# Kernel optimization log

Measured on AMD Instinct MI355X. Metric: run time of the kernel, lower is better.

## Reference

```python
import jax, jax.numpy as jnp
import numpy as np

B, C, H, W = 8, 256, 128, 128
HEADS, DIM_HEAD = 4, 32
HID = HEADS * DIM_HEAD  # 128


def setup_inputs() -> dict:
    key = jax.random.key(0)
    k1, k2, k3, k4 = jax.random.split(key, 4)
    x = jax.random.normal(k1, (B, C, H, W), dtype=jnp.float32)
    # 1x1 conv weights stored as [out_ch, in_ch]
    w_qkv = jax.random.normal(k2, (3 * HID, C), dtype=jnp.float32) * (1.0 / np.sqrt(C))
    w_out = jax.random.normal(k3, (C, HID), dtype=jnp.float32) * (1.0 / np.sqrt(HID))
    b_out = jax.random.normal(k4, (C,), dtype=jnp.float32) * 0.01
    return {"x": x, "w_qkv": w_qkv, "w_out": w_out, "b_out": b_out}


def reference(x, w_qkv, w_out, b_out):
    b, c, h, w = x.shape
    n = h * w
    # 1x1 conv == channel matmul
    qkv = jnp.einsum('oc,bchw->bohw', w_qkv, x)  # [b, 3*HID, h, w]
    q, k, v = jnp.split(qkv, 3, axis=1)
    # rearrange 'b (heads d) h w -> b heads d (h w)'
    def to_heads(t):
        return t.reshape(b, HEADS, DIM_HEAD, n)
    q, k, v = to_heads(q), to_heads(k), to_heads(v)
    k = jax.nn.softmax(k, axis=-1)  # over spatial n
    # q_scale is False: q used as-is
    context = jnp.einsum('bhdn,bhen->bhde', k, v)   # [b, heads, d, e] small
    out = jnp.einsum('bhde,bhdn->bhen', context, q)  # [b, heads, e, n]
    out = out.reshape(b, HID, h, w)
    out = jnp.einsum('oc,bchw->bohw', w_out, out) + b_out[None, :, None, None]
    return out
```

## Files before the change

### kernel.cpp

```cpp
#include <hip/hip_runtime.h>
#include <stdint.h>

#define BB 8
#define CIN 256
#define NSP 16384
#define HID 128

typedef __bf16 bfrag __attribute__((ext_vector_type(8)));
typedef float  f32x4 __attribute__((ext_vector_type(4)));

__device__ __forceinline__ unsigned short f2bf(float f) {
  union { float f; unsigned int u; } v; v.f = f;
  unsigned int u = v.u;
  return (unsigned short)((u + 0x7FFFu + ((u >> 16) & 1u)) >> 16);
}

__global__ __launch_bounds__(512, 2) void la_fused(const float* __restrict__ x,
                                                   const float* __restrict__ w_qkv,
                                                   unsigned short* __restrict__ qT,
                                                   float* __restrict__ ctxp,
                                                   float* __restrict__ sums) {
  __shared__ __align__(16) union {
    struct { unsigned short Wt[384][40]; unsigned short Xb[128][40]; } g;
    struct { unsigned short Lk[64][136]; unsigned short Lv[64][136];
             float Pc[4][1024]; } e;
  } sh;
  const int chunk = blockIdx.x;
  const int n0 = chunk * 128;
  const int b = blockIdx.y;
  const int t = threadIdx.x;
  const int lane = t & 63, wv = t >> 6;
  const int l15 = lane & 15, q = lane >> 4;
  const int cl = t & 31;
  const int n16 = (t >> 5) * 8;
  const float* xp = x + (size_t)b * CIN * NSP + n0;
  f32x4 acc[3][8];
#pragma unroll
  for (int i = 0; i < 3; ++i)
#pragma unroll
    for (int j = 0; j < 8; ++j) acc[i][j] = 0.0f;

  for (int kc = 0; kc < 8; ++kc) {
#pragma unroll
    for (int i = 0; i < 3; ++i) {
      const int id = t + i * 512;
      const int row = id >> 2, c8 = (id & 3) * 8;
      const float* wr = w_qkv + (size_t)row * CIN + kc * 32 + c8;
      const float4 wa = *(const float4*)wr;
      const float4 wb4 = *(const float4*)(wr + 4);
      ushort4 p0, p1;
      p0.x = f2bf(wa.x); p0.y = f2bf(wa.y); p0.z = f2bf(wa.z); p0.w = f2bf(wa.w);
      p1.x = f2bf(wb4.x); p1.y = f2bf(wb4.y); p1.z = f2bf(wb4.z); p1.w = f2bf(wb4.w);
      *(ushort4*)&sh.g.Wt[row][c8] = p0;
      *(ushort4*)&sh.g.Wt[row][c8 + 4] = p1;
    }
    const float* xr = xp + (size_t)(kc * 32 + cl) * NSP + n16;
    const float4 xa = *(const float4*)xr;
    const float4 xb4 = *(const float4*)(xr + 4);
    sh.g.Xb[n16 + 0][cl] = f2bf(xa.x);
    sh.g.Xb[n16 + 1][cl] = f2bf(xa.y);
    sh.g.Xb[n16 + 2][cl] = f2bf(xa.z);
    sh.g.Xb[n16 + 3][cl] = f2bf(xa.w);
    sh.g.Xb[n16 + 4][cl] = f2bf(xb4.x);
    sh.g.Xb[n16 + 5][cl] = f2bf(xb4.y);
    sh.g.Xb[n16 + 6][cl] = f2bf(xb4.z);
    sh.g.Xb[n16 + 7][cl] = f2bf(xb4.w);
    __syncthreads();
    bfrag a0 = *(const bfrag*)&sh.g.Wt[wv * 16 + l15][q * 8];
    bfrag a1 = *(const bfrag*)&sh.g.Wt[128 + wv * 16 + l15][q * 8];
    bfrag a2 = *(const bfrag*)&sh.g.Wt[256 + wv * 16 + l15][q * 8];
    bfrag bb[8];
#pragma unroll
    for (int ni = 0; ni < 8; ++ni) bb[ni] = *(const bfrag*)&sh.g.Xb[ni * 16 + l15][q * 8];
#pragma unroll
    for (int ni = 0; ni < 8; ++ni) {
      acc[0][ni] = __builtin_amdgcn_mfma_f32_16x16x32_bf16(a0, bb[ni], acc[0][ni], 0, 0, 0);
      acc[1][ni] = __builtin_amdgcn_mfma_f32_16x16x32_bf16(a1, bb[ni], acc[1][ni], 0, 0, 0);
      acc[2][ni] = __builtin_amdgcn_mfma_f32_16x16x32_bf16(a2, bb[ni], acc[2][ni], 0, 0, 0);
    }
    __syncthreads();
  }

  {
    unsigned short* qb = qT + (size_t)b * NSP * HID;
    const int qrow = wv * 16 + q * 4;
#pragma unroll
    for (int ni = 0; ni < 8; ++ni) {
      const int n = n0 + ni * 16 + l15;
      ushort4 pk;
      pk.x = f2bf(acc[0][ni][0]);
      pk.y = f2bf(acc[0][ni][1]);
      pk.z = f2bf(acc[0][ni][2]);
      pk.w = f2bf(acc[0][ni][3]);
      *(ushort4*)(qb + (size_t)n * HID + qrow) = pk;
    }
  }
  {
    float sp[4] = {0.f, 0.f, 0.f, 0.f};
#pragma unroll
    for (int ni = 0; ni < 8; ++ni)
#pragma unroll
      for (int rg = 0; rg < 4; ++rg) sp[rg] += __expf(acc[1][ni][rg]);
#pragma unroll
    for (int rg = 0; rg < 4; ++rg) {
      float s = sp[rg];
      s += __shfl_down(s, 8, 16);
      s += __shfl_down(s, 4, 16);
      s += __shfl_down(s, 2, 16);
      s += __shfl_down(s, 1, 16);
      if (l15 == 0) atomicAdd(&sums[b * 128 + wv * 16 + q * 4 + rg], s);
    }
  }
  float* cp = ctxp + ((size_t)chunk * 32 + b * 4) * 1024;
#pragma unroll
  for (int ph = 0; ph < 2; ++ph) {
    if ((wv >> 2) == ph) {
      const int r = (wv & 3) * 16 + q * 4;
#pragma unroll
      for (int ni = 0; ni < 8; ++ni)
#pragma unroll
        for (int rg = 0; rg < 4; ++rg) {
          sh.e.Lk[r + rg][ni * 16 + l15] = f2bf(__expf(acc[1][ni][rg]));
          sh.e.Lv[r + rg][ni * 16 + l15] = f2bf(acc[2][ni][rg]);
        }
    }
    __syncthreads();
    const int hl = wv >> 2, nq = wv & 3;
    f32x4 c2[2][2];
    c2[0][0] = 0.f; c2[0][1] = 0.f; c2[1][0] = 0.f; c2[1][1] = 0.f;
    bfrag ka[2], vb[2];
#pragma unroll
    for (int d2 = 0; d2 < 2; ++d2)
      ka[d2] = *(const bfrag*)&sh.e.Lk[hl * 32 + d2 * 16 + l15][nq * 32 + q * 8];
#pragma unroll
    for (int e2 = 0; e2 < 2; ++e2)
      vb[e2] = *(const bfrag*)&sh.e.Lv[hl * 32 + e2 * 16 + l15][nq * 32 + q * 8];
#pragma unroll
    for (int d2 = 0; d2 < 2; ++d2)
#pragma unroll
      for (int e2 = 0; e2 < 2; ++e2)
        c2[d2][e2] = __builtin_amdgcn_mfma_f32_16x16x32_bf16(ka[d2], vb[e2], c2[d2][e2], 0, 0, 0);
    const int slot = hl * 2 + (nq & 1);
    if (nq < 2) {
#pragma unroll
      for (int d2 = 0; d2 < 2; ++d2)
#pragma unroll
        for (int e2 = 0; e2 < 2; ++e2)
#pragma unroll
          for (int rg = 0; rg < 4; ++rg)
            sh.e.Pc[slot][(d2 * 16 + q * 4 + rg) * 32 + e2 * 16 + l15] = c2[d2][e2][rg];
    }
    __syncthreads();
    if (nq >= 2) {
#pragma unroll
      for (int d2 = 0; d2 < 2; ++d2)
#pragma unroll
        for (int e2 = 0; e2 < 2; ++e2)
#pragma unroll
          for (int rg = 0; rg < 4; ++rg)
            sh.e.Pc[slot][(d2 * 16 + q * 4 + rg) * 32 + e2 * 16 + l15] += c2[d2][e2][rg];
    }
    __syncthreads();
    for (int idx = t; idx < 2048; idx += 512) {
      const int h2 = idx >> 10, pos = idx & 1023;
      cp[(ph * 2 + h2) * 1024 + pos] = sh.e.Pc[h2 * 2][pos] + sh.e.Pc[h2 * 2 + 1][pos];
    }
    __syncthreads();
  }
}

__global__ __launch_bounds__(256) void la_reduce(const float* __restrict__ ctxp,
                                                 float* __restrict__ ctxu) {
  const int gid = blockIdx.x * 256 + threadIdx.x;
  float s = 0.f;
#pragma unroll 8
  for (int c = 0; c < 128; ++c) s += ctxp[(size_t)c * 32768 + gid];
  ctxu[gid] = s;
}

__global__ __launch_bounds__(128) void la_weff(const float* __restrict__ w_out,
                                               const float* __restrict__ ctxu,
                                               const float* __restrict__ sums,
                                               unsigned short* __restrict__ weff) {
  const int o = blockIdx.x;
  const int b = blockIdx.y;
  const int cp = threadIdx.x;
  const int h = cp >> 5, d = cp & 31;
  const float* wrow = w_out + (size_t)o * HID + h * 32;
  const float* crow = ctxu + ((size_t)(b * 4 + h) * 32 + d) * 32;
  float s = 0.f;
#pragma unroll 8
  for (int e = 0; e < 32; ++e) s += wrow[e] * crow[e];
  s *= (1.0f / sums[b * 128 + h * 32 + d]);
  weff[((size_t)b * 256 + o) * HID + cp] = f2bf(s);
}

__global__ __launch_bounds__(256) void la_out_gemm(const unsigned short* __restrict__ weff,
                                                   const unsigned short* __restrict__ qT,
                                                   const float* __restrict__ b_out,
                                                   float* __restrict__ out) {
  __shared__ __align__(16) unsigned short At[128][40];
  __shared__ __align__(16) unsigned short Bt[128][40];
  const int mblk = blockIdx.x;
  const int n0 = blockIdx.y * 128;
  const int b = blockIdx.z;
  const int t = threadIdx.x;
  const int lane = t & 63, wv = t >> 6;
  const int wm = (wv >> 1) * 64, wn = (wv & 1) * 64;
  const int l15 = lane & 15, q = lane >> 4;
  f32x4 acc[4][4];
#pragma unroll
  for (int i = 0; i < 4; ++i)
#pragma unroll
    for (int j = 0; j < 4; ++j) acc[i][j] = 0.0f;
  const unsigned short* abase = weff + ((size_t)b * 256 + mblk * 128) * HID;
  const unsigned short* bbase = qT + ((size_t)b * NSP + n0) * HID;
  const int r = t >> 1, hh = (t & 1) * 16;
  for (int kc = 0; kc < 4; ++kc) {
    const int ko = kc * 32 + hh;
    uint4 a0 = *(const uint4*)(abase + (size_t)r * HID + ko);
    uint4 a1 = *(const uint4*)(abase + (size_t)r * HID + ko + 8);
    uint4 b0 = *(const uint4*)(bbase + (size_t)r * HID + ko);
    uint4 b1 = *(const uint4*)(bbase + (size_t)r * HID + ko + 8);
    *(uint4*)&At[r][hh] = a0;
    *(uint4*)&At[r][hh + 8] = a1;
    *(uint4*)&Bt[r][hh] = b0;
    *(uint4*)&Bt[r][hh + 8] = b1;
    __syncthreads();
    bfrag a[4], bf[4];
#pragma unroll
    for (int mi = 0; mi < 4; ++mi) a[mi] = *(const bfrag*)&At[wm + mi * 16 + l15][q * 8];
#pragma unroll
    for (int ni = 0; ni < 4; ++ni) bf[ni] = *(const bfrag*)&Bt[wn + ni * 16 + l15][q * 8];
#pragma unroll
    for (int mi = 0; mi < 4; ++mi)
#pragma unroll
      for (int ni = 0; ni < 4; ++ni)
        acc[mi][ni] = __builtin_amdgcn_mfma_f32_16x16x32_bf16(a[mi], bf[ni], acc[mi][ni], 0, 0, 0);
    __syncthreads();
  }
  float* obase = out + ((size_t)b * 256 + mblk * 128) * NSP;
#pragma unroll
  for (int mi = 0; mi < 4; ++mi) {
    const int ob = wm + mi * 16 + q * 4;
    const float4 bias = *(const float4*)(b_out + mblk * 128 + ob);
    float ba[4] = {bias.x, bias.y, bias.z, bias.w};
#pragma unroll
    for (int ni = 0; ni < 4; ++ni) {
      const int n = n0 + wn + ni * 16 + l15;
#pragma unroll
      for (int rg = 0; rg < 4; ++rg)
        obase[(size_t)(ob + rg) * NSP + n] = acc[mi][ni][rg] + ba[rg];
    }
  }
}


extern "C" void kernel_launch(void* const* d_in, const int* in_sizes, int n_in,
                              void* d_out, int out_size, void* d_ws, size_t ws_size,
                              hipStream_t stream) {
  (void)in_sizes; (void)n_in; (void)out_size; (void)ws_size;
  const float* x     = (const float*)d_in[0];
  const float* w_qkv = (const float*)d_in[1];
  const float* w_out = (const float*)d_in[2];
  const float* b_out = (const float*)d_in[3];
  float* out = (float*)d_out;
  char* ws = (char*)d_ws;
  unsigned short* qT   = (unsigned short*)(ws);
  float* ctxp          = (float*)(ws + 33554432);
  float* ctxu          = (float*)(ws + 50331648);
  float* sums          = (float*)(ws + 50462720);
  unsigned short* weff = (unsigned short*)(ws + 50466816);

  hipMemsetAsync(sums, 0, 4096, stream);
  la_fused<<<dim3(NSP / 128, BB), dim3(512), 0, stream>>>(x, w_qkv, qT, ctxp, sums);
  la_reduce<<<dim3(128), dim3(256), 0, stream>>>(ctxp, ctxu);
  la_weff<<<dim3(256, BB), dim3(128), 0, stream>>>(w_out, ctxu, sums, weff);
  la_out_gemm<<<dim3(2, NSP / 128, BB), dim3(256), 0, stream>>>(weff, qT, b_out, out);
}
```

Measured before the change: 342.7 us.

## Fold q projection into combined output weight and pre-transpose x to bf16

The q projection is no longer computed and stored. Instead a per-batch combined weight (w_out·context/sums·w_q) is formed and applied directly to x in a final GEMM. x is transposed and cast to bf16 once, so both GEMM kernels can use global_load_lds staging, and the per-chunk context partials are reduced with atomics instead of a separate reduce kernel. This drops the qT round trip and the reduce pass, at the cost of an extra transpose kernel, a larger K=256 final GEMM, and atomic contention on ctxu.

```diff
diff --git a/kernel.cpp b/kernel.cpp
--- a/kernel.cpp
+++ b/kernel.cpp
@@ -15,13 +15,52 @@
   return (unsigned short)((u + 0x7FFFu + ((u >> 16) & 1u)) >> 16);
 }
 
-__global__ __launch_bounds__(512, 2) void la_fused(const float* __restrict__ x,
-                                                   const float* __restrict__ w_qkv,
-                                                   unsigned short* __restrict__ qT,
-                                                   float* __restrict__ ctxp,
-                                                   float* __restrict__ sums) {
+#define GLL16(gp, lp)                                                              \
+  __builtin_amdgcn_global_load_lds((const __attribute__((address_space(1))) void*)(gp), \
+                                   (__attribute__((address_space(3))) void*)(lp), 16, 0, 0)
+
+__global__ __launch_bounds__(256) void la_cast_w(const float* __restrict__ w,
+                                                 unsigned short* __restrict__ wb, int n) {
+  int i = blockIdx.x * 256 + threadIdx.x;
+  if (i < n) wb[i] = f2bf(w[i]);
+}
+
+__global__ __launch_bounds__(256) void la_transpose(const float* __restrict__ x,
+                                                    unsigned short* __restrict__ xT) {
+  __shared__ __align__(16) float tile[64][68];
+  const int n0 = blockIdx.x * 64;
+  const int c0 = blockIdx.y * 64;
+  const int b  = blockIdx.z;
+  const int t = threadIdx.x;
+  const float* xp = x + (size_t)b * CIN * NSP;
+  const int nseg = (t & 15) * 4;
+  const int crow = t >> 4;
+#pragma unroll
+  for (int i = 0; i < 4; ++i) {
+    const int c = crow + i * 16;
+    const float4 v = *(const float4*)(xp + (size_t)(c0 + c) * NSP + n0 + nseg);
+    tile[nseg + 0][c] = v.x;
+    tile[nseg + 1][c] = v.y;
+    tile[nseg + 2][c] = v.z;
+    tile[nseg + 3][c] = v.w;
+  }
+  __syncthreads();
+  const int n = t >> 2;
+  const int seg = (t & 3) * 16;
+  unsigned short* op = xT + ((size_t)b * NSP + n0 + n) * CIN + c0 + seg;
+  union { unsigned short u[16]; uint4 q[2]; } pk;
+#pragma unroll
+  for (int k = 0; k < 16; ++k) pk.u[k] = f2bf(tile[n][seg + k]);
+  *(uint4*)(op) = pk.q[0];
+  *(uint4*)(op + 8) = pk.q[1];
+}
+
+__global__ __launch_bounds__(512) void la_kv_ctx(const unsigned short* __restrict__ wkv,
+                                                 const unsigned short* __restrict__ xT,
+                                                 float* __restrict__ ctxu,
+                                                 float* __restrict__ sums) {
   __shared__ __align__(16) union {
-    struct { unsigned short Wt[384][40]; unsigned short Xb[128][40]; } g;
+    struct { unsigned short Wt[256][32]; unsigned short Xt[128][32]; } g;
     struct { unsigned short Lk[64][136]; unsigned short Lv[64][136];
              float Pc[4][1024]; } e;
   } sh;
@@ -31,76 +70,39 @@
   const int t = threadIdx.x;
   const int lane = t & 63, wv = t >> 6;
   const int l15 = lane & 15, q = lane >> 4;
-  const int cl = t & 31;
-  const int n16 = (t >> 5) * 8;
-  const float* xp = x + (size_t)b * CIN * NSP + n0;
-  f32x4 acc[3][8];
-#pragma unroll
-  for (int i = 0; i < 3; ++i)
+  const int wbase = (t & 0x1C0) * 16;
+  const int grow = t >> 2, gseg = (t & 3) * 8;
+  f32x4 acc[2][8];
+#pragma unroll
+  for (int i = 0; i < 2; ++i)
 #pragma unroll
     for (int j = 0; j < 8; ++j) acc[i][j] = 0.0f;
-
+  const unsigned short* xbase = xT + ((size_t)b * NSP + n0) * CIN;
   for (int kc = 0; kc < 8; ++kc) {
-#pragma unroll
-    for (int i = 0; i < 3; ++i) {
-      const int id = t + i * 512;
-      const int row = id >> 2, c8 = (id & 3) * 8;
-      const float* wr = w_qkv + (size_t)row * CIN + kc * 32 + c8;
-      const float4 wa = *(const float4*)wr;
-      const float4 wb4 = *(const float4*)(wr + 4);
-      ushort4 p0, p1;
-      p0.x = f2bf(wa.x); p0.y = f2bf(wa.y); p0.z = f2bf(wa.z); p0.w = f2bf(wa.w);
-      p1.x = f2bf(wb4.x); p1.y = f2bf(wb4.y); p1.z = f2bf(wb4.z); p1.w = f2bf(wb4.w);
-      *(ushort4*)&sh.g.Wt[row][c8] = p0;
-      *(ushort4*)&sh.g.Wt[row][c8 + 4] = p1;
-    }
-    const float* xr = xp + (size_t)(kc * 32 + cl) * NSP + n16;
-    const float4 xa = *(const float4*)xr;
-    const float4 xb4 = *(const float4*)(xr + 4);
-    sh.g.Xb[n16 + 0][cl] = f2bf(xa.x);
-    sh.g.Xb[n16 + 1][cl] = f2bf(xa.y);
-    sh.g.Xb[n16 + 2][cl] = f2bf(xa.z);
-    sh.g.Xb[n16 + 3][cl] = f2bf(xa.w);
-    sh.g.Xb[n16 + 4][cl] = f2bf(xb4.x);
-    sh.g.Xb[n16 + 5][cl] = f2bf(xb4.y);
-    sh.g.Xb[n16 + 6][cl] = f2bf(xb4.z);
-    sh.g.Xb[n16 + 7][cl] = f2bf(xb4.w);
+    __syncthreads();
+    const int ko = kc * 32 + gseg;
+    GLL16(wkv + (size_t)grow * CIN + ko,          (char*)sh.g.Wt + wbase);
+    GLL16(wkv + (size_t)(grow + 128) * CIN + ko,  (char*)sh.g.Wt + 8192 + wbase);
+    GLL16(xbase + (size_t)grow * CIN + ko,        (char*)sh.g.Xt + wbase);
     __syncthreads();
     bfrag a0 = *(const bfrag*)&sh.g.Wt[wv * 16 + l15][q * 8];
     bfrag a1 = *(const bfrag*)&sh.g.Wt[128 + wv * 16 + l15][q * 8];
-    bfrag a2 = *(const bfrag*)&sh.g.Wt[256 + wv * 16 + l15][q * 8];
     bfrag bb[8];
 #pragma unroll
-    for (int ni = 0; ni < 8; ++ni) bb[ni] = *(const bfrag*)&sh.g.Xb[ni * 16 + l15][q * 8];
+    for (int ni = 0; ni < 8; ++ni) bb[ni] = *(const bfrag*)&sh.g.Xt[ni * 16 + l15][q * 8];
 #pragma unroll
     for (int ni = 0; ni < 8; ++ni) {
       acc[0][ni] = __builtin_amdgcn_mfma_f32_16x16x32_bf16(a0, bb[ni], acc[0][ni], 0, 0, 0);
       acc[1][ni] = __builtin_amdgcn_mfma_f32_16x16x32_bf16(a1, bb[ni], acc[1][ni], 0, 0, 0);
-      acc[2][ni] = __builtin_amdgcn_mfma_f32_16x16x32_bf16(a2, bb[ni], acc[2][ni], 0, 0, 0);
-    }
-    __syncthreads();
-  }
-
-  {
-    unsigned short* qb = qT + (size_t)b * NSP * HID;
-    const int qrow = wv * 16 + q * 4;
-#pragma unroll
-    for (int ni = 0; ni < 8; ++ni) {
-      const int n = n0 + ni * 16 + l15;
-      ushort4 pk;
-      pk.x = f2bf(acc[0][ni][0]);
-      pk.y = f2bf(acc[0][ni][1]);
-      pk.z = f2bf(acc[0][ni][2]);
-      pk.w = f2bf(acc[0][ni][3]);
-      *(ushort4*)(qb + (size_t)n * HID + qrow) = pk;
-    }
-  }
+    }
+  }
+  __syncthreads();
   {
     float sp[4] = {0.f, 0.f, 0.f, 0.f};
 #pragma unroll
     for (int ni = 0; ni < 8; ++ni)
 #pragma unroll
-      for (int rg = 0; rg < 4; ++rg) sp[rg] += __expf(acc[1][ni][rg]);
+      for (int rg = 0; rg < 4; ++rg) sp[rg] += __expf(acc[0][ni][rg]);
 #pragma unroll
     for (int rg = 0; rg < 4; ++rg) {
       float s = sp[rg];
@@ -111,7 +113,6 @@
       if (l15 == 0) atomicAdd(&sums[b * 128 + wv * 16 + q * 4 + rg], s);
     }
   }
-  float* cp = ctxp + ((size_t)chunk * 32 + b * 4) * 1024;
 #pragma unroll
   for (int ph = 0; ph < 2; ++ph) {
     if ((wv >> 2) == ph) {
@@ -120,8 +121,8 @@
       for (int ni = 0; ni < 8; ++ni)
 #pragma unroll
         for (int rg = 0; rg < 4; ++rg) {
-          sh.e.Lk[r + rg][ni * 16 + l15] = f2bf(__expf(acc[1][ni][rg]));
-          sh.e.Lv[r + rg][ni * 16 + l15] = f2bf(acc[2][ni][rg]);
+          sh.e.Lk[r + rg][ni * 16 + l15] = f2bf(__expf(acc[0][ni][rg]));
+          sh.e.Lv[r + rg][ni * 16 + l15] = f2bf(acc[1][ni][rg]);
         }
     }
     __syncthreads();
@@ -163,94 +164,89 @@
     __syncthreads();
     for (int idx = t; idx < 2048; idx += 512) {
       const int h2 = idx >> 10, pos = idx & 1023;
-      cp[(ph * 2 + h2) * 1024 + pos] = sh.e.Pc[h2 * 2][pos] + sh.e.Pc[h2 * 2 + 1][pos];
-    }
-    __syncthreads();
-  }
-}
-
-__global__ __launch_bounds__(256) void la_reduce(const float* __restrict__ ctxp,
-                                                 float* __restrict__ ctxu) {
-  const int gid = blockIdx.x * 256 + threadIdx.x;
-  float s = 0.f;
-#pragma unroll 8
-  for (int c = 0; c < 128; ++c) s += ctxp[(size_t)c * 32768 + gid];
-  ctxu[gid] = s;
-}
-
-__global__ __launch_bounds__(128) void la_weff(const float* __restrict__ w_out,
-                                               const float* __restrict__ ctxu,
-                                               const float* __restrict__ sums,
-                                               unsigned short* __restrict__ weff) {
+      atomicAdd(&ctxu[((size_t)(b * 4 + ph * 2 + h2)) * 1024 + pos],
+                sh.e.Pc[h2 * 2][pos] + sh.e.Pc[h2 * 2 + 1][pos]);
+    }
+    __syncthreads();
+  }
+}
+
+__global__ __launch_bounds__(256) void la_wcomb(const float* __restrict__ w_out,
+                                                const float* __restrict__ w_qkv,
+                                                const float* __restrict__ ctxu,
+                                                const float* __restrict__ sums,
+                                                unsigned short* __restrict__ wcomb) {
+  __shared__ float Weff_l[128];
   const int o = blockIdx.x;
   const int b = blockIdx.y;
-  const int cp = threadIdx.x;
-  const int h = cp >> 5, d = cp & 31;
-  const float* wrow = w_out + (size_t)o * HID + h * 32;
-  const float* crow = ctxu + ((size_t)(b * 4 + h) * 32 + d) * 32;
-  float s = 0.f;
+  const int t = threadIdx.x;
+  if (t < 128) {
+    const int h = t >> 5, d = t & 31;
+    const float* wrow = w_out + (size_t)o * HID + h * 32;
+    const float* crow = ctxu + ((size_t)(b * 4 + h) * 32 + d) * 32;
+    float s = 0.f;
 #pragma unroll 8
-  for (int e = 0; e < 32; ++e) s += wrow[e] * crow[e];
-  s *= (1.0f / sums[b * 128 + h * 32 + d]);
-  weff[((size_t)b * 256 + o) * HID + cp] = f2bf(s);
-}
-
-__global__ __launch_bounds__(256) void la_out_gemm(const unsigned short* __restrict__ weff,
-                                                   const unsigned short* __restrict__ qT,
-                                                   const float* __restrict__ b_out,
-                                                   float* __restrict__ out) {
-  __shared__ __align__(16) unsigned short At[128][40];
-  __shared__ __align__(16) unsigned short Bt[128][40];
-  const int mblk = blockIdx.x;
-  const int n0 = blockIdx.y * 128;
-  const int b = blockIdx.z;
+    for (int e = 0; e < 32; ++e) s += wrow[e] * crow[e];
+    Weff_l[t] = s / sums[b * 128 + t];
+  }
+  __syncthreads();
+  float a = 0.f;
+#pragma unroll 8
+  for (int cp = 0; cp < 128; ++cp) a += Weff_l[cp] * w_qkv[(size_t)cp * CIN + t];
+  wcomb[((size_t)b * 256 + o) * 256 + t] = f2bf(a);
+}
+
+__global__ __launch_bounds__(512) void la_final(const unsigned short* __restrict__ wcomb,
+                                                const unsigned short* __restrict__ xT,
+                                                const float* __restrict__ b_out,
+                                                float* __restrict__ out) {
+  __shared__ __align__(16) unsigned short Wt[256][32];
+  __shared__ __align__(16) unsigned short Xt[128][32];
+  const int chunk = blockIdx.x;
+  const int n0 = chunk * 128;
+  const int b = blockIdx.y;
   const int t = threadIdx.x;
   const int lane = t & 63, wv = t >> 6;
-  const int wm = (wv >> 1) * 64, wn = (wv & 1) * 64;
   const int l15 = lane & 15, q = lane >> 4;
-  f32x4 acc[4][4];
-#pragma unroll
-  for (int i = 0; i < 4; ++i)
-#pragma unroll
-    for (int j = 0; j < 4; ++j) acc[i][j] = 0.0f;
-  const unsigned short* abase = weff + ((size_t)b * 256 + mblk * 128) * HID;
-  const unsigned short* bbase = qT + ((size_t)b * NSP + n0) * HID;
-  const int r = t >> 1, hh = (t & 1) * 16;
-  for (int kc = 0; kc < 4; ++kc) {
-    const int ko = kc * 32 + hh;
-    uint4 a0 = *(const uint4*)(abase + (size_t)r * HID + ko);
-    uint4 a1 = *(const uint4*)(abase + (size_t)r * HID + ko + 8);
-    uint4 b0 = *(const uint4*)(bbase + (size_t)r * HID + ko);
-    uint4 b1 = *(const uint4*)(bbase + (size_t)r * HID + ko + 8);
-    *(uint4*)&At[r][hh] = a0;
-    *(uint4*)&At[r][hh + 8] = a1;
-    *(uint4*)&Bt[r][hh] = b0;
-    *(uint4*)&Bt[r][hh + 8] = b1;
-    __syncthreads();
-    bfrag a[4], bf[4];
-#pragma unroll
-    for (int mi = 0; mi < 4; ++mi) a[mi] = *(const bfrag*)&At[wm + mi * 16 + l15][q * 8];
-#pragma unroll
-    for (int ni = 0; ni < 4; ++ni) bf[ni] = *(const bfrag*)&Bt[wn + ni * 16 + l15][q * 8];
-#pragma unroll
-    for (int mi = 0; mi < 4; ++mi)
-#pragma unroll
-      for (int ni = 0; ni < 4; ++ni)
-        acc[mi][ni] = __builtin_amdgcn_mfma_f32_16x16x32_bf16(a[mi], bf[ni], acc[mi][ni], 0, 0, 0);
-    __syncthreads();
-  }
-  float* obase = out + ((size_t)b * 256 + mblk * 128) * NSP;
-#pragma unroll
-  for (int mi = 0; mi < 4; ++mi) {
-    const int ob = wm + mi * 16 + q * 4;
-    const float4 bias = *(const float4*)(b_out + mblk * 128 + ob);
+  const int wbase = (t & 0x1C0) * 16;
+  const int grow = t >> 2, gseg = (t & 3) * 8;
+  f32x4 acc[2][8];
+#pragma unroll
+  for (int i = 0; i < 2; ++i)
+#pragma unroll
+    for (int j = 0; j < 8; ++j) acc[i][j] = 0.0f;
+  const unsigned short* abase = wcomb + (size_t)b * 256 * 256;
+  const unsigned short* xbase = xT + ((size_t)b * NSP + n0) * CIN;
+  for (int kc = 0; kc < 8; ++kc) {
+    __syncthreads();
+    const int ko = kc * 32 + gseg;
+    GLL16(abase + (size_t)grow * 256 + ko,        (char*)Wt + wbase);
+    GLL16(abase + (size_t)(grow + 128) * 256 + ko, (char*)Wt + 8192 + wbase);
+    GLL16(xbase + (size_t)grow * CIN + ko,        (char*)Xt + wbase);
+    __syncthreads();
+    bfrag a0 = *(const bfrag*)&Wt[wv * 16 + l15][q * 8];
+    bfrag a1 = *(const bfrag*)&Wt[128 + wv * 16 + l15][q * 8];
+    bfrag bb[8];
+#pragma unroll
+    for (int ni = 0; ni < 8; ++ni) bb[ni] = *(const bfrag*)&Xt[ni * 16 + l15][q * 8];
+#pragma unroll
+    for (int ni = 0; ni < 8; ++ni) {
+      acc[0][ni] = __builtin_amdgcn_mfma_f32_16x16x32_bf16(a0, bb[ni], acc[0][ni], 0, 0, 0);
+      acc[1][ni] = __builtin_amdgcn_mfma_f32_16x16x32_bf16(a1, bb[ni], acc[1][ni], 0, 0, 0);
+    }
+  }
+  float* obase = out + (size_t)b * 256 * NSP;
+#pragma unroll
+  for (int band = 0; band < 2; ++band) {
+    const int ob = band * 128 + wv * 16 + q * 4;
+    const float4 bias = *(const float4*)(b_out + ob);
     float ba[4] = {bias.x, bias.y, bias.z, bias.w};
 #pragma unroll
-    for (int ni = 0; ni < 4; ++ni) {
-      const int n = n0 + wn + ni * 16 + l15;
+    for (int ni = 0; ni < 8; ++ni) {
+      const int n = n0 + ni * 16 + l15;
 #pragma unroll
       for (int rg = 0; rg < 4; ++rg)
-        obase[(size_t)(ob + rg) * NSP + n] = acc[mi][ni][rg] + ba[rg];
+        obase[(size_t)(ob + rg) * NSP + n] = acc[band][ni][rg] + ba[rg];
     }
   }
 }
@@ -266,15 +262,16 @@
   const float* b_out = (const float*)d_in[3];
   float* out = (float*)d_out;
   char* ws = (char*)d_ws;
-  unsigned short* qT   = (unsigned short*)(ws);
-  float* ctxp          = (float*)(ws + 33554432);
-  float* ctxu          = (float*)(ws + 50331648);
-  float* sums          = (float*)(ws + 50462720);
-  unsigned short* weff = (unsigned short*)(ws + 50466816);
-
-  hipMemsetAsync(sums, 0, 4096, stream);
-  la_fused<<<dim3(NSP / 128, BB), dim3(512), 0, stream>>>(x, w_qkv, qT, ctxp, sums);
-  la_reduce<<<dim3(128), dim3(256), 0, stream>>>(ctxp, ctxu);
-  la_weff<<<dim3(256, BB), dim3(128), 0, stream>>>(w_out, ctxu, sums, weff);
-  la_out_gemm<<<dim3(2, NSP / 128, BB), dim3(256), 0, stream>>>(weff, qT, b_out, out);
-}
+  unsigned short* xT    = (unsigned short*)(ws);
+  unsigned short* wqb2  = (unsigned short*)(ws + 67108864);
+  unsigned short* wcomb = (unsigned short*)(ws + 67239936);
+  float* ctxu           = (float*)(ws + 68288512);
+  float* sums           = (float*)(ws + 68419584);
+
+  hipMemsetAsync(ctxu, 0, 131072 + 4096, stream);
+  la_cast_w<<<dim3(256), dim3(256), 0, stream>>>(w_qkv + 128 * CIN, wqb2, 256 * CIN);
+  la_transpose<<<dim3(NSP / 64, CIN / 64, BB), dim3(256), 0, stream>>>(x, xT);
+  la_kv_ctx<<<dim3(NSP / 128, BB), dim3(512), 0, stream>>>(wqb2, xT, ctxu, sums);
+  la_wcomb<<<dim3(256, BB), dim3(256), 0, stream>>>(w_out, w_qkv, ctxu, sums, wcomb);
+  la_final<<<dim3(NSP / 128, BB), dim3(512), 0, stream>>>(wcomb, xT, b_out, out);
+}
```

Measured after the change: 354.5 us. 1.03x slower.
